# Kernel tuning notes

Measured on AMD Instinct MI355X. Metric: run time of the kernel, lower is better.

The kernel has to match this reference:

```python
import jax, jax.numpy as jnp
import numpy as np

RADIUS, HMIN, HMAX, NSAMPLE = 0.05, -0.02, 0.04, 32
EPS = 1e-5


def setup_inputs() -> dict:
    key = jax.random.key(0)
    ks = jax.random.split(key, 6)
    B, N, C, OUT = 4, 2048, 256, 256
    seed_xyz_graspable = jax.random.uniform(ks[0], (B, N, 3), jnp.float32) * 0.2
    seed_features_graspable = jax.random.normal(ks[1], (B, C, N), jnp.float32)
    vp_rot = jax.random.normal(ks[2], (B, N, 3, 3), jnp.float32)
    W1 = jax.random.normal(ks[3], (OUT, 3 + C), jnp.float32) * 0.02
    W2 = jax.random.normal(ks[4], (OUT, OUT), jnp.float32) * 0.02
    return {
        "seed_xyz_graspable": seed_xyz_graspable,
        "seed_features_graspable": seed_features_graspable,
        "vp_rot": vp_rot,
        "W1": W1, "gamma1": jnp.ones((OUT,), jnp.float32), "beta1": jnp.zeros((OUT,), jnp.float32),
        "W2": W2, "gamma2": jnp.ones((OUT,), jnp.float32), "beta2": jnp.zeros((OUT,), jnp.float32),
    }


def _cylinder_query(xyz, rot):
    # xyz: (B,N,3), rot: (B,N,3,3); new_xyz == xyz.
    B, N, _ = xyz.shape
    d = xyz[:, None, :, :] - xyz[:, :, None, :]                  # (B,P,N,3) offsets to each candidate
    r = jnp.einsum('bpij,bpnj->bpni', rot, d)                    # rotate into cylinder frame (rot @ d)
    mask = (r[..., 1] ** 2 + r[..., 2] ** 2 < RADIUS ** 2) & (r[..., 0] > HMIN) & (r[..., 0] < HMAX)
    order = jnp.arange(N, dtype=jnp.int32)
    keys = jnp.where(mask, order, order + N)                     # in-cylinder points sort first, stable order
    _, idx = jax.lax.top_k(-keys, NSAMPLE)                       # first NSAMPLE indices satisfying the query
    valid = jnp.take_along_axis(mask, idx, axis=-1)
    first = idx[..., :1]
    any_valid = valid[..., :1]
    idx = jnp.where(valid, idx, jnp.where(any_valid, first, 0))  # pad with first hit like the CUDA kernel
    return idx                                                   # (B,P,NSAMPLE) int32


def _group(xyz, features, rot, idx):
    gxyz = jax.vmap(lambda a, i: a[i])(xyz, idx)                 # (B,P,S,3)
    gxyz = (gxyz - xyz[:, :, None, :]) / RADIUS                  # center on query + normalize_xyz
    gxyz = jnp.einsum('bpsj,bpjk->bpsk', gxyz, rot)              # rotate_xyz: grouped_xyz @ rot
    gfeat = jax.vmap(lambda f, i: f[:, i])(features, idx)        # (B,C,P,S)
    return jnp.concatenate([gxyz.transpose(0, 3, 1, 2), gfeat], axis=1)  # (B,3+C,P,S)


def _conv_bn_relu(x, W, gamma, beta):
    y = jnp.einsum('oc,bcps->bops', W, x)                        # 1x1 conv, no bias (bn=True)
    mu = y.mean(axis=(0, 2, 3), keepdims=True)
    var = y.var(axis=(0, 2, 3), keepdims=True)
    y = (y - mu) * jax.lax.rsqrt(var + EPS)
    y = y * gamma[None, :, None, None] + beta[None, :, None, None]
    return jax.nn.relu(y)


def reference(seed_xyz_graspable, seed_features_graspable, vp_rot, W1, gamma1, beta1, W2, gamma2, beta2):
    idx = _cylinder_query(seed_xyz_graspable, vp_rot)
    g = _group(seed_xyz_graspable, seed_features_graspable, vp_rot, idx)
    h = _conv_bn_relu(g, W1, gamma1, beta1)
    h = _conv_bn_relu(h, W2, gamma2, beta2)
    return h.max(axis=3)                                         # maxpool over nsample -> (B,OUT,P)
```

## Files before the change

kernel.cpp:

```cpp
#include <hip/hip_runtime.h>

typedef unsigned short u16;
typedef unsigned int u32;
typedef __attribute__((ext_vector_type(8))) short bf16x8;
typedef __attribute__((ext_vector_type(4))) float f32x4;

#define NPTS 2048
#define CFEAT 256
#define NS 32
#define MTOT 262144
#define NBLK 4096
#define INV_N (1.0f/262144.0f)

__device__ __forceinline__ float bf2f(u16 u) {
    union { u32 i; float f; } v; v.i = ((u32)u) << 16; return v.f;
}
__device__ __forceinline__ u16 f2bf(float f) {
    union { float f; u32 i; } v; v.f = f;
    u32 i = v.i;
    return (u16)((i + 0x7fffu + ((i >> 16) & 1u)) >> 16);
}
__device__ __forceinline__ u32 pk2bf(float a, float b) {
    u32 r;
    asm("v_cvt_pk_bf16_f32 %0, %1, %2" : "=v"(r) : "v"(a), "v"(b));
    return r;
}

__device__ __forceinline__ void gload16(const void* g, void* l) {
    __builtin_amdgcn_global_load_lds((const __attribute__((address_space(1))) void*)g,
                                     (__attribute__((address_space(3))) void*)l, 16, 0, 0);
}

__global__ __launch_bounds__(256) void query_k(const float* __restrict__ xyz, const float* __restrict__ rot,
                                               const float* __restrict__ feat,
                                               int* __restrict__ idx, u16* __restrict__ gxyz,
                                               u16* __restrict__ featT,
                                               const float* __restrict__ W1, const float* __restrict__ W2,
                                               u16* __restrict__ Wp1, u16* __restrict__ Wp2) {
    __shared__ float sm[32 * 33];
    __shared__ float xbs[NPTS * 3];
    __shared__ int sidx[4 * NS];
    const int tid = threadIdx.x;
    if (blockIdx.x < 256) {
        int o = blockIdx.x;
        Wp1[o * 288 + tid] = f2bf(W1[o * 259 + 3 + tid]);
        if (tid < 32) Wp1[o * 288 + 256 + tid] = (tid < 3) ? f2bf(W1[o * 259 + tid]) : (u16)0;
        Wp2[o * 256 + tid] = f2bf(W2[o * 256 + tid]);
    }
    const int b = blockIdx.x >> 9;
    const float* xb = xyz + (size_t)b * NPTS * 3;
    const int c0 = ((blockIdx.x >> 6) & 7) * 32;
    const int n0f = (blockIdx.x & 63) * 32;
    {
        int x = tid & 31, y = tid >> 5;
        #pragma unroll
        for (int rr = 0; rr < 4; rr++) {
            int c = c0 + y + rr * 8;
            sm[(y + rr * 8) * 33 + x] = feat[((size_t)(b * CFEAT + c)) * NPTS + n0f + x];
        }
    }
    {
        const uint4* src = (const uint4*)xb;
        uint4* dst = (uint4*)xbs;
        #pragma unroll
        for (int u = 0; u < 6; u++) dst[u * 256 + tid] = src[u * 256 + tid];
    }
    __syncthreads();
    {
        int x = tid & 31, y = tid >> 5;
        #pragma unroll
        for (int rr = 0; rr < 4; rr++) {
            int n = n0f + y + rr * 8;
            featT[((size_t)(b * NPTS + n)) * CFEAT + c0 + x] = (u16)pk2bf(sm[x * 33 + (y + rr * 8)], 0.f);
        }
    }
    const int wid = tid >> 6;
    const int pid = blockIdx.x * 4 + wid;
    const int lane = tid & 63;
    const int p = pid & 2047;
    float px = xbs[p * 3 + 0], py = xbs[p * 3 + 1], pz = xbs[p * 3 + 2];
    const float* rp = rot + (size_t)pid * 9;
    float r00 = rp[0], r01 = rp[1], r02 = rp[2];
    float r10 = rp[3], r11 = rp[4], r12 = rp[5];
    float r20 = rp[6], r21 = rp[7], r22 = rp[8];
    int cnt = 0, first = 0;
    for (int n0 = 0; n0 < NPTS && cnt < NS; n0 += 64) {
        int n = n0 + lane;
        float dx = __fsub_rn(xbs[n * 3 + 0], px);
        float dy = __fsub_rn(xbs[n * 3 + 1], py);
        float dz = __fsub_rn(xbs[n * 3 + 2], pz);
        float a0 = __fadd_rn(__fadd_rn(__fmul_rn(r00, dx), __fmul_rn(r01, dy)), __fmul_rn(r02, dz));
        float a1 = __fadd_rn(__fadd_rn(__fmul_rn(r10, dx), __fmul_rn(r11, dy)), __fmul_rn(r12, dz));
        float a2 = __fadd_rn(__fadd_rn(__fmul_rn(r20, dx), __fmul_rn(r21, dy)), __fmul_rn(r22, dz));
        float t2 = __fadd_rn(__fmul_rn(a1, a1), __fmul_rn(a2, a2));
        bool valid = (t2 < 0.0025f) && (a0 > -0.02f) && (a0 < 0.04f);
        unsigned long long bal = __ballot(valid);
        if (cnt == 0 && bal) first = n0 + __builtin_ctzll(bal);
        int rank = __builtin_popcountll(bal & ((1ull << lane) - 1ull));
        int slot = cnt + rank;
        if (valid && slot < NS) sidx[wid * NS + slot] = n;
        cnt += __builtin_popcountll(bal);
    }
    int filled = cnt < NS ? cnt : NS;
    __syncthreads();
    if (lane < NS) {
        int i = (lane < filled) ? sidx[wid * NS + lane] : (cnt > 0 ? first : 0);
        idx[(size_t)pid * NS + lane] = i;
        float dx = (xbs[i * 3 + 0] - px) * 20.0f;
        float dy = (xbs[i * 3 + 1] - py) * 20.0f;
        float dz = (xbs[i * 3 + 2] - pz) * 20.0f;
        float g0 = dx * r00 + dy * r10 + dz * r20;
        float g1 = dx * r01 + dy * r11 + dz * r21;
        float g2 = dx * r02 + dy * r12 + dz * r22;
        uint2 v;
        v.x = pk2bf(g0, g1);
        v.y = pk2bf(g2, 0.f);
        *(uint2*)(gxyz + ((size_t)pid * NS + lane) * 4) = v;
    }
}

template <int FULL, int STORE>
__global__ __launch_bounds__(256) void fused_k(
    const u16* __restrict__ featT, const u16* __restrict__ gxyz, const int* __restrict__ idx,
    const u16* __restrict__ Wp1, const u16* __restrict__ Wp2, const float* __restrict__ ab1,
    float* __restrict__ psum, float* __restrict__ psq,
    float* __restrict__ ymax, float* __restrict__ ymin, uint2* __restrict__ y1f)
{
    __shared__ __attribute__((aligned(16))) u16 As[64 * 64];
    __shared__ __attribute__((aligned(16))) u16 Bs[256 * 64];
    __shared__ __attribute__((aligned(16))) u16 y1s[FULL ? 64 * 264 : 16];
    __shared__ int rowbase_s[64];

    const int tid = threadIdx.x;
    const int lane = tid & 63, wave = tid >> 6;
    const int quad = lane >> 4, tl = lane & 15;
    const int bx = blockIdx.x;
    const int m0 = bx * 64;

    if (tid < 64) {
        int m = m0 + tid;
        int gi = idx[m];
        int b = m >> 16;
        rowbase_s[tid] = (b * NPTS + gi) * CFEAT;
    }
    __syncthreads();

    const int sr8 = tid >> 3;
    const int koffA = (((tid & 7) ^ (sr8 & 7)) * 8);

    f32x4 acc[4][4];
    #pragma unroll
    for (int i = 0; i < 4; i++)
        #pragma unroll
        for (int j = 0; j < 4; j++) acc[i][j] = (f32x4){0.f, 0.f, 0.f, 0.f};

    for (int t = 0; t < 4; t++) {
        const int k0 = t * 64;
        __syncthreads();
        gload16(featT + rowbase_s[sr8] + k0 + koffA, As + tid * 8);
        gload16(featT + rowbase_s[sr8 + 32] + k0 + koffA, As + 2048 + tid * 8);
        #pragma unroll
        for (int c = 0; c < 8; c++)
            gload16(Wp1 + (c * 32 + sr8) * 288 + k0 + koffA, Bs + c * 2048 + tid * 8);
        __syncthreads();
        #pragma unroll
        for (int kk = 0; kk < 2; kk++) {
            bf16x8 af[4], bv[4];
            #pragma unroll
            for (int i = 0; i < 4; i++)
                af[i] = *(const bf16x8*)(As + (i * 16 + tl) * 64 + (((kk * 4 + quad) ^ (tl & 7)) * 8));
            #pragma unroll
            for (int j = 0; j < 4; j++)
                bv[j] = *(const bf16x8*)(Bs + (j * 64 + wave * 16 + tl) * 64 + (((kk * 4 + quad) ^ (tl & 7)) * 8));
            #pragma unroll
            for (int i = 0; i < 4; i++)
                #pragma unroll
                for (int j = 0; j < 4; j++)
                    acc[i][j] = __builtin_amdgcn_mfma_f32_16x16x32_bf16(af[i], bv[j], acc[i][j], 0, 0, 0);
        }
    }
    {
        __syncthreads();
        const int srow = tid >> 2, sc16 = tid & 3;
        uint4 va = make_uint4(0, 0, 0, 0);
        if (sc16 == 0) {
            uint2 g2 = *(const uint2*)(gxyz + (size_t)(m0 + srow) * 4);
            va.x = g2.x; va.y = g2.y;
        }
        *(uint4*)(As + srow * 64 + ((sc16 ^ (srow & 7)) * 8)) = va;
        #pragma unroll
        for (int s = 0; s < 4; s++) {
            uint4 w = *(const uint4*)(Wp1 + tid * 288 + 256 + s * 8);
            *(uint4*)(Bs + tid * 64 + ((s ^ (tid & 7)) * 8)) = w;
        }
        __syncthreads();
        bf16x8 af[4], bv[4];
        #pragma unroll
        for (int i = 0; i < 4; i++)
            af[i] = *(const bf16x8*)(As + (i * 16 + tl) * 64 + ((quad ^ (tl & 7)) * 8));
        #pragma unroll
        for (int j = 0; j < 4; j++)
            bv[j] = *(const bf16x8*)(Bs + (j * 64 + wave * 16 + tl) * 64 + ((quad ^ (tl & 7)) * 8));
        #pragma unroll
        for (int i = 0; i < 4; i++)
            #pragma unroll
            for (int j = 0; j < 4; j++)
                acc[i][j] = __builtin_amdgcn_mfma_f32_16x16x32_bf16(af[i], bv[j], acc[i][j], 0, 0, 0);
    }

    if (!FULL) {
        #pragma unroll
        for (int j = 0; j < 4; j++) {
            float s = 0.f, q2 = 0.f;
            #pragma unroll
            for (int i = 0; i < 4; i++) {
                float v0 = acc[i][j][0], v1 = acc[i][j][1], v2 = acc[i][j][2], v3 = acc[i][j][3];
                if (STORE) {
                    u32 lo = pk2bf(v0, v1);
                    u32 hi = pk2bf(v2, v3);
                    y1f[((size_t)(bx * 4 + wave) * 16 + i * 4 + j) * 64 + lane] = make_uint2(lo, hi);
                    v0 = bf2f((u16)(lo & 0xffff)); v1 = bf2f((u16)(lo >> 16));
                    v2 = bf2f((u16)(hi & 0xffff)); v3 = bf2f((u16)(hi >> 16));
                }
                s += v0 + v1 + v2 + v3;
                q2 += v0 * v0 + v1 * v1 + v2 * v2 + v3 * v3;
            }
            s += __shfl_xor(s, 16); s += __shfl_xor(s, 32);
            q2 += __shfl_xor(q2, 16); q2 += __shfl_xor(q2, 32);
            if (quad == 0) {
                int col = j * 64 + wave * 16 + tl;
                psum[(size_t)bx * 256 + col] = s;
                psq[(size_t)bx * 256 + col] = q2;
            }
        }
        return;
    }

    #pragma unroll
    for (int j = 0; j < 4; j++) {
        int col = j * 64 + wave * 16 + tl;
        float a = ab1[col], bb = ab1[256 + col];
        #pragma unroll
        for (int i = 0; i < 4; i++)
            #pragma unroll
            for (int r = 0; r < 4; r++) {
                float v = fmaxf(fmaf(acc[i][j][r], a, bb), 0.f);
                y1s[(i * 16 + quad * 4 + r) * 264 + col] = f2bf(v);
            }
    }

    const int srow = tid >> 2, sc16 = tid & 3;
    f32x4 acc2[4][4];
    #pragma unroll
    for (int i = 0; i < 4; i++)
        #pragma unroll
        for (int j = 0; j < 4; j++) acc2[i][j] = (f32x4){0.f, 0.f, 0.f, 0.f};
    for (int ks = 0; ks < 8; ks++) {
        const int k0 = ks * 32;
        __syncthreads();
        #pragma unroll
        for (int q = 0; q < 4; q++)
            gload16(Wp2 + (srow + q * 64) * 256 + k0 + sc16 * 8, Bs + q * 2048 + tid * 8);
        __syncthreads();
        bf16x8 af[4], bv[4];
        #pragma unroll
        for (int i = 0; i < 4; i++) af[i] = *(const bf16x8*)(y1s + (i * 16 + tl) * 264 + k0 + quad * 8);
        #pragma unroll
        for (int j = 0; j < 4; j++) bv[j] = *(const bf16x8*)(Bs + (j * 64 + wave * 16 + tl) * 32 + quad * 8);
        #pragma unroll
        for (int i = 0; i < 4; i++)
            #pragma unroll
            for (int j = 0; j < 4; j++)
                acc2[i][j] = __builtin_amdgcn_mfma_f32_16x16x32_bf16(af[i], bv[j], acc2[i][j], 0, 0, 0);
    }

    #pragma unroll
    for (int j = 0; j < 4; j++) {
        int col = j * 64 + wave * 16 + tl;
        float s = 0.f, q2 = 0.f;
        float mx0 = -3.0e38f, mn0 = 3.0e38f, mx1 = -3.0e38f, mn1 = 3.0e38f;
        #pragma unroll
        for (int i = 0; i < 4; i++)
            #pragma unroll
            for (int r = 0; r < 4; r++) {
                float v = acc2[i][j][r];
                s += v; q2 += v * v;
                if (i < 2) { mx0 = fmaxf(mx0, v); mn0 = fminf(mn0, v); }
                else       { mx1 = fmaxf(mx1, v); mn1 = fminf(mn1, v); }
            }
        s += __shfl_xor(s, 16); s += __shfl_xor(s, 32);
        q2 += __shfl_xor(q2, 16); q2 += __shfl_xor(q2, 32);
        mx0 = fmaxf(mx0, __shfl_xor(mx0, 16)); mx0 = fmaxf(mx0, __shfl_xor(mx0, 32));
        mn0 = fminf(mn0, __shfl_xor(mn0, 16)); mn0 = fminf(mn0, __shfl_xor(mn0, 32));
        mx1 = fmaxf(mx1, __shfl_xor(mx1, 16)); mx1 = fmaxf(mx1, __shfl_xor(mx1, 32));
        mn1 = fminf(mn1, __shfl_xor(mn1, 16)); mn1 = fminf(mn1, __shfl_xor(mn1, 32));
        if (quad == 0) {
            psum[(size_t)bx * 256 + col] = s;
            psq[(size_t)bx * 256 + col] = q2;
            size_t p0 = (size_t)(bx * 2) * 256 + col;
            size_t p1 = (size_t)(bx * 2 + 1) * 256 + col;
            ymax[p0] = mx0; ymin[p0] = mn0;
            ymax[p1] = mx1; ymin[p1] = mn1;
        }
    }
}

__global__ __launch_bounds__(256) void fused2_k(
    const uint2* __restrict__ y1f, const u16* __restrict__ Wp2, const float* __restrict__ ab1,
    float* __restrict__ psum, float* __restrict__ psq,
    float* __restrict__ ymax, float* __restrict__ ymin)
{
    __shared__ __attribute__((aligned(16))) u16 Bs[256 * 64];
    __shared__ __attribute__((aligned(16))) u16 y1s[64 * 136];
    const int tid = threadIdx.x;
    const int lane = tid & 63, wave = tid >> 6;
    const int quad = lane >> 4, tl = lane & 15;
    const int bx = blockIdx.x;
    const int sr8 = tid >> 3;
    const int koffB = (((tid & 7) ^ (sr8 & 7)) * 8);

    float yv[4][4][4];
    #pragma unroll
    for (int j = 0; j < 4; j++) {
        int col = j * 64 + wave * 16 + tl;
        float a = ab1[col], bb = ab1[256 + col];
        #pragma unroll
        for (int i = 0; i < 4; i++) {
            uint2 v = y1f[((size_t)(bx * 4 + wave) * 16 + i * 4 + j) * 64 + lane];
            yv[j][i][0] = fmaxf(fmaf(bf2f((u16)(v.x & 0xffff)), a, bb), 0.f);
            yv[j][i][1] = fmaxf(fmaf(bf2f((u16)(v.x >> 16)), a, bb), 0.f);
            yv[j][i][2] = fmaxf(fmaf(bf2f((u16)(v.y & 0xffff)), a, bb), 0.f);
            yv[j][i][3] = fmaxf(fmaf(bf2f((u16)(v.y >> 16)), a, bb), 0.f);
        }
    }
    #pragma unroll
    for (int j = 0; j < 2; j++) {
        int col = j * 64 + wave * 16 + tl;
        #pragma unroll
        for (int i = 0; i < 4; i++)
            #pragma unroll
            for (int r = 0; r < 4; r++)
                y1s[(i * 16 + quad * 4 + r) * 136 + col] = (u16)pk2bf(yv[j][i][r], 0.f);
    }

    f32x4 acc2[4][4];
    #pragma unroll
    for (int i = 0; i < 4; i++)
        #pragma unroll
        for (int j = 0; j < 4; j++) acc2[i][j] = (f32x4){0.f, 0.f, 0.f, 0.f};

    for (int t = 0; t < 4; t++) {
        const int k0 = t * 64;
        __syncthreads();
        if (t == 2) {
            #pragma unroll
            for (int j = 2; j < 4; j++) {
                int lc = (j - 2) * 64 + wave * 16 + tl;
                #pragma unroll
                for (int i = 0; i < 4; i++)
                    #pragma unroll
                    for (int r = 0; r < 4; r++)
                        y1s[(i * 16 + quad * 4 + r) * 136 + lc] = (u16)pk2bf(yv[j][i][r], 0.f);
            }
        }
        #pragma unroll
        for (int c = 0; c < 8; c++)
            gload16(Wp2 + (c * 32 + sr8) * 256 + k0 + koffB, Bs + c * 2048 + tid * 8);
        __syncthreads();
        const int klb = (t & 1) * 64;
        #pragma unroll
        for (int kk = 0; kk < 2; kk++) {
            bf16x8 af[4], bv[4];
            #pragma unroll
            for (int i = 0; i < 4; i++)
                af[i] = *(const bf16x8*)(y1s + (i * 16 + tl) * 136 + klb + kk * 32 + quad * 8);
            #pragma unroll
            for (int j = 0; j < 4; j++)
                bv[j] = *(const bf16x8*)(Bs + (j * 64 + wave * 16 + tl) * 64 + (((kk * 4 + quad) ^ (tl & 7)) * 8));
            #pragma unroll
            for (int i = 0; i < 4; i++)
                #pragma unroll
                for (int j = 0; j < 4; j++)
                    acc2[i][j] = __builtin_amdgcn_mfma_f32_16x16x32_bf16(af[i], bv[j], acc2[i][j], 0, 0, 0);
        }
    }

    #pragma unroll
    for (int j = 0; j < 4; j++) {
        int col = j * 64 + wave * 16 + tl;
        float s = 0.f, q2 = 0.f;
        float mx0 = -3.0e38f, mn0 = 3.0e38f, mx1 = -3.0e38f, mn1 = 3.0e38f;
        #pragma unroll
        for (int i = 0; i < 4; i++)
            #pragma unroll
            for (int r = 0; r < 4; r++) {
                float v = acc2[i][j][r];
                s += v; q2 += v * v;
                if (i < 2) { mx0 = fmaxf(mx0, v); mn0 = fminf(mn0, v); }
                else       { mx1 = fmaxf(mx1, v); mn1 = fminf(mn1, v); }
            }
        s += __shfl_xor(s, 16); s += __shfl_xor(s, 32);
        q2 += __shfl_xor(q2, 16); q2 += __shfl_xor(q2, 32);
        mx0 = fmaxf(mx0, __shfl_xor(mx0, 16)); mx0 = fmaxf(mx0, __shfl_xor(mx0, 32));
        mn0 = fminf(mn0, __shfl_xor(mn0, 16)); mn0 = fminf(mn0, __shfl_xor(mn0, 32));
        mx1 = fmaxf(mx1, __shfl_xor(mx1, 16)); mx1 = fmaxf(mx1, __shfl_xor(mx1, 32));
        mn1 = fminf(mn1, __shfl_xor(mn1, 16)); mn1 = fminf(mn1, __shfl_xor(mn1, 32));
        if (quad == 0) {
            psum[(size_t)bx * 256 + col] = s;
            psq[(size_t)bx * 256 + col] = q2;
            size_t p0 = (size_t)(bx * 2) * 256 + col;
            size_t p1 = (size_t)(bx * 2 + 1) * 256 + col;
            ymax[p0] = mx0; ymin[p0] = mn0;
            ymax[p1] = mx1; ymin[p1] = mn1;
        }
    }
}

__global__ __launch_bounds__(256) void reduce1_k(const float* __restrict__ psum, const float* __restrict__ psq,
                                                 float* __restrict__ ps2, float* __restrict__ pq2) {
    int j = blockIdx.x, t = threadIdx.x;
    float s = 0.f, q = 0.f;
    #pragma unroll 4
    for (int kk = 0; kk < 64; kk++) {
        size_t r = (size_t)(j * 64 + kk) * 256 + t;
        s += psum[r]; q += psq[r];
    }
    ps2[j * 256 + t] = s;
    pq2[j * 256 + t] = q;
}

__global__ __launch_bounds__(256) void reduce2_k(const float* __restrict__ ps2, const float* __restrict__ pq2,
                                                 const float* __restrict__ gamma, const float* __restrict__ beta,
                                                 float* __restrict__ ab) {
    int c = threadIdx.x;
    float S = 0.f, Q = 0.f;
    for (int j = 0; j < 64; j++) {
        S += ps2[j * 256 + c];
        Q += pq2[j * 256 + c];
    }
    float mu = S * INV_N;
    float var = Q * INV_N - mu * mu;
    float a = gamma[c] * rsqrtf(var + 1e-5f);
    ab[c] = a;
    ab[256 + c] = beta[c] - mu * a;
}

__global__ __launch_bounds__(256) void final_k(const float* __restrict__ ymax, const float* __restrict__ ymin,
                                               const float* __restrict__ ab, float* __restrict__ out) {
    __shared__ float sm[32 * 33];
    int b = blockIdx.z;
    int n0 = blockIdx.x * 32, o0 = blockIdx.y * 32;
    int t = threadIdx.x, x = t & 31, y = t >> 5;
    #pragma unroll
    for (int rr = 0; rr < 4; rr++) {
        int n = n0 + y + rr * 8;
        int o = o0 + x;
        float a = ab[o], bb = ab[256 + o];
        size_t p = (size_t)(b * NPTS + n) * 256 + o;
        float v = (a >= 0.f) ? ymax[p] : ymin[p];
        sm[(y + rr * 8) * 33 + x] = fmaxf(fmaf(v, a, bb), 0.f);
    }
    __syncthreads();
    #pragma unroll
    for (int rr = 0; rr < 4; rr++)
        out[((size_t)(b * 256 + o0 + y + rr * 8)) * NPTS + n0 + x] = sm[x * 33 + (y + rr * 8)];
}

extern "C" void kernel_launch(void* const* d_in, const int* in_sizes, int n_in,
                              void* d_out, int out_size, void* d_ws, size_t ws_size,
                              hipStream_t stream) {
    const float* xyz    = (const float*)d_in[0];
    const float* feat   = (const float*)d_in[1];
    const float* rot    = (const float*)d_in[2];
    const float* W1     = (const float*)d_in[3];
    const float* gamma1 = (const float*)d_in[4];
    const float* beta1  = (const float*)d_in[5];
    const float* W2     = (const float*)d_in[6];
    const float* gamma2 = (const float*)d_in[7];
    const float* beta2  = (const float*)d_in[8];
    float* out = (float*)d_out;

    char* ws = (char*)d_ws;
    u16*   featT = (u16*)(ws + 0);
    int*   idxp  = (int*)(ws + 4194304);
    u16*   gxyz  = (u16*)(ws + 5242880);
    u16*   Wp1   = (u16*)(ws + 7340032);
    u16*   Wp2   = (u16*)(ws + 7487488);
    float* ab1   = (float*)(ws + 7618560);
    float* ab2   = (float*)(ws + 7620608);
    float* psum  = (float*)(ws + 7622656);
    float* psq   = (float*)(ws + 11816960);
    float* ymax  = (float*)(ws + 16011264);
    float* ymin  = (float*)(ws + 24399872);
    uint2* y1f   = (uint2*)(ws + 32788480);
    const size_t BIG_NEED = 32788480ull + 134217728ull;

    float* r1s = (float*)(ws + 24399872);
    float* r1q = r1s + 16384;
    float* r2s = (float*)(ws + 5242880);
    float* r2q = r2s + 16384;

    query_k<<<2048, 256, 0, stream>>>(xyz, rot, feat, idxp, gxyz, featT, W1, W2, Wp1, Wp2);

    if (ws_size >= BIG_NEED) {
        fused_k<0, 1><<<NBLK, 256, 0, stream>>>(featT, gxyz, idxp, Wp1, Wp2, ab1, psum, psq, ymax, ymin, y1f);
        reduce1_k<<<64, 256, 0, stream>>>(psum, psq, r1s, r1q);
        reduce2_k<<<1, 256, 0, stream>>>(r1s, r1q, gamma1, beta1, ab1);
        fused2_k<<<NBLK, 256, 0, stream>>>(y1f, Wp2, ab1, psum, psq, ymax, ymin);
        reduce1_k<<<64, 256, 0, stream>>>(psum, psq, r2s, r2q);
        reduce2_k<<<1, 256, 0, stream>>>(r2s, r2q, gamma2, beta2, ab2);
    } else {
        fused_k<0, 0><<<NBLK, 256, 0, stream>>>(featT, gxyz, idxp, Wp1, Wp2, ab1, psum, psq, ymax, ymin, nullptr);
        reduce1_k<<<64, 256, 0, stream>>>(psum, psq, r1s, r1q);
        reduce2_k<<<1, 256, 0, stream>>>(r1s, r1q, gamma1, beta1, ab1);
        fused_k<1, 0><<<NBLK, 256, 0, stream>>>(featT, gxyz, idxp, Wp1, Wp2, ab1, psum, psq, ymax, ymin, nullptr);
        reduce1_k<<<64, 256, 0, stream>>>(psum, psq, r2s, r2q);
        reduce2_k<<<1, 256, 0, stream>>>(r2s, r2q, gamma2, beta2, ab2);
    }
    final_k<<<dim3(64, 8, 4), 256, 0, stream>>>(ymax, ymin, ab2, out);
}
```

Baseline: 228.8 us.

## Compute BN1 statistics from per-point GEMM with gather histogram instead of full pass

BN1 statistics are computed algebraically. A histogram counts how often each source point is gathered and sums its grouped xyz. A small GEMM over the 8192 unique points (instead of 262144 grouped rows) then weights the feature projection by those counts, and cross terms with the xyz part come from second moments. The separate first-pass kernel and its large bf16 intermediate buffer are dropped. A single fused kernel recomputes layer 1 and runs layer 2 with a smaller shared-memory footprint. The risks are float atomics in shared memory and precision loss in the var = E[x²] − mu² form.

```diff
diff --git a/kernel.cpp b/kernel.cpp
--- a/kernel.cpp
+++ b/kernel.cpp
@@ -10,6 +10,7 @@
 #define NS 32
 #define MTOT 262144
 #define NBLK 4096
+#define NROW 8192
 #define INV_N (1.0f/262144.0f)
 
 __device__ __forceinline__ float bf2f(u16 u) {
@@ -119,17 +120,161 @@
     }
 }
 
-template <int FULL, int STORE>
-__global__ __launch_bounds__(256) void fused_k(
+__global__ __launch_bounds__(256) void hist_k(const int* __restrict__ idx, const u16* __restrict__ gxyz,
+                                              float* __restrict__ hpart, float* __restrict__ xst64,
+                                              float* __restrict__ Sacc) {
+    __shared__ float hist[8192];
+    __shared__ float red[9 * 4];
+    const int t = threadIdx.x, lane = t & 63, wave = t >> 6;
+    const int g = blockIdx.x;
+    const int base = g * 4096;
+    if (g == 0) { Sacc[t] = 0.f; Sacc[t + 256] = 0.f; Sacc[t + 512] = 0.f; }
+    for (int i = t; i < 8192; i += 256) hist[i] = 0.f;
+    __syncthreads();
+    float p[9] = {0.f,0.f,0.f,0.f,0.f,0.f,0.f,0.f,0.f};
+    for (int u = 0; u < 16; u++) {
+        int m = base + u * 256 + t;
+        int r = idx[m];
+        uint2 v = *(const uint2*)(gxyz + (size_t)m * 4);
+        float x0 = bf2f((u16)(v.x & 0xffff));
+        float x1 = bf2f((u16)(v.x >> 16));
+        float x2 = bf2f((u16)(v.y & 0xffff));
+        atomicAdd(hist + r * 4 + 0, 1.f);
+        atomicAdd(hist + r * 4 + 1, x0);
+        atomicAdd(hist + r * 4 + 2, x1);
+        atomicAdd(hist + r * 4 + 3, x2);
+        p[0] += x0; p[1] += x1; p[2] += x2;
+        p[3] += x0 * x0; p[4] += x0 * x1; p[5] += x0 * x2;
+        p[6] += x1 * x1; p[7] += x1 * x2; p[8] += x2 * x2;
+    }
+    __syncthreads();
+    for (int i = t; i < 8192; i += 256) hpart[(size_t)g * 8192 + i] = hist[i];
+    #pragma unroll
+    for (int k = 0; k < 9; k++) {
+        float s = p[k];
+        #pragma unroll
+        for (int o = 1; o < 64; o <<= 1) s += __shfl_xor(s, o);
+        if (lane == 0) red[k * 4 + wave] = s;
+    }
+    __syncthreads();
+    if (t < 9) xst64[g * 9 + t] = red[t * 4 + 0] + red[t * 4 + 1] + red[t * 4 + 2] + red[t * 4 + 3];
+}
+
+__global__ __launch_bounds__(256) void zgemm_k(const u16* __restrict__ featT, const u16* __restrict__ Wp1,
+                                               const float* __restrict__ hpart,
+                                               float* __restrict__ Sacc, float* __restrict__ Qacc,
+                                               float* __restrict__ Xacc) {
+    __shared__ __attribute__((aligned(16))) u16 As[64 * 32];
+    __shared__ __attribute__((aligned(16))) u16 Bs[256 * 32];
+    __shared__ float cxs[64 * 4];
+    const int tid = threadIdx.x;
+    const int lane = tid & 63, wave = tid >> 6;
+    const int quad = lane >> 4, tl = lane & 15;
+    const int m0 = blockIdx.x * 64;
+    const int srow = tid >> 2, sc16 = tid & 3;
+    const int abase = (m0 + srow) * CFEAT + sc16 * 8;
+
+    {
+        const int b = m0 >> 11;
+        const int rl0 = m0 & 2047;
+        int row = tid >> 2, c = tid & 3;
+        float s = 0.f;
+        #pragma unroll
+        for (int sg = 0; sg < 16; sg++)
+            s += hpart[(size_t)(b * 16 + sg) * 8192 + (rl0 + row) * 4 + c];
+        cxs[tid] = s;
+    }
+
+    f32x4 acc[4][4];
+    #pragma unroll
+    for (int i = 0; i < 4; i++)
+        #pragma unroll
+        for (int j = 0; j < 4; j++) acc[i][j] = (f32x4){0.f, 0.f, 0.f, 0.f};
+
+    for (int ks = 0; ks < 8; ks++) {
+        const int k0 = ks * 32;
+        __syncthreads();
+        gload16(featT + abase + k0, As + tid * 8);
+        #pragma unroll
+        for (int q = 0; q < 4; q++)
+            gload16(Wp1 + (srow + q * 64) * 288 + k0 + sc16 * 8, Bs + q * 2048 + tid * 8);
+        __syncthreads();
+        bf16x8 af[4], bv[4];
+        #pragma unroll
+        for (int i = 0; i < 4; i++) af[i] = *(const bf16x8*)(As + (i * 16 + tl) * 32 + quad * 8);
+        #pragma unroll
+        for (int j = 0; j < 4; j++) bv[j] = *(const bf16x8*)(Bs + (wave * 64 + j * 16 + tl) * 32 + quad * 8);
+        #pragma unroll
+        for (int i = 0; i < 4; i++)
+            #pragma unroll
+            for (int j = 0; j < 4; j++)
+                acc[i][j] = __builtin_amdgcn_mfma_f32_16x16x32_bf16(af[i], bv[j], acc[i][j], 0, 0, 0);
+    }
+
+    #pragma unroll
+    for (int j = 0; j < 4; j++) {
+        int col = wave * 64 + j * 16 + tl;
+        float wx0 = bf2f(Wp1[col * 288 + 256]);
+        float wx1 = bf2f(Wp1[col * 288 + 257]);
+        float wx2 = bf2f(Wp1[col * 288 + 258]);
+        float S = 0.f, Q = 0.f, X = 0.f;
+        #pragma unroll
+        for (int i = 0; i < 4; i++)
+            #pragma unroll
+            for (int rr = 0; rr < 4; rr++) {
+                int row = i * 16 + quad * 4 + rr;
+                float4 cx = *(const float4*)(cxs + row * 4);
+                float z = acc[i][j][rr];
+                S += cx.x * z;
+                Q += cx.x * z * z;
+                X += z * (wx0 * cx.y + wx1 * cx.z + wx2 * cx.w);
+            }
+        S += __shfl_xor(S, 16); S += __shfl_xor(S, 32);
+        Q += __shfl_xor(Q, 16); Q += __shfl_xor(Q, 32);
+        X += __shfl_xor(X, 16); X += __shfl_xor(X, 32);
+        if (quad == 0) {
+            atomicAdd(Sacc + col, S);
+            atomicAdd(Qacc + col, Q);
+            atomicAdd(Xacc + col, X);
+        }
+    }
+}
+
+__global__ __launch_bounds__(256) void ab1_k(const float* __restrict__ Sacc, const float* __restrict__ Qacc,
+                                             const float* __restrict__ Xacc, const float* __restrict__ xst64,
+                                             const u16* __restrict__ Wp1,
+                                             const float* __restrict__ gamma, const float* __restrict__ beta,
+                                             float* __restrict__ ab) {
+    int c = threadIdx.x;
+    float xs[9] = {0.f,0.f,0.f,0.f,0.f,0.f,0.f,0.f,0.f};
+    for (int g = 0; g < 64; g++)
+        #pragma unroll
+        for (int k = 0; k < 9; k++) xs[k] += xst64[g * 9 + k];
+    float wx0 = bf2f(Wp1[c * 288 + 256]);
+    float wx1 = bf2f(Wp1[c * 288 + 257]);
+    float wx2 = bf2f(Wp1[c * 288 + 258]);
+    float S = Sacc[c] + wx0 * xs[0] + wx1 * xs[1] + wx2 * xs[2];
+    float qxx = wx0 * wx0 * xs[3] + wx1 * wx1 * xs[6] + wx2 * wx2 * xs[8]
+              + 2.f * (wx0 * wx1 * xs[4] + wx0 * wx2 * xs[5] + wx1 * wx2 * xs[7]);
+    float Q = Qacc[c] + 2.f * Xacc[c] + qxx;
+    float mu = S * INV_N;
+    float var = Q * INV_N - mu * mu;
+    float a = gamma[c] * rsqrtf(var + 1e-5f);
+    ab[c] = a;
+    ab[256 + c] = beta[c] - mu * a;
+}
+
+__global__ __launch_bounds__(256) void full_k(
     const u16* __restrict__ featT, const u16* __restrict__ gxyz, const int* __restrict__ idx,
     const u16* __restrict__ Wp1, const u16* __restrict__ Wp2, const float* __restrict__ ab1,
     float* __restrict__ psum, float* __restrict__ psq,
-    float* __restrict__ ymax, float* __restrict__ ymin, uint2* __restrict__ y1f)
+    float* __restrict__ ymax, float* __restrict__ ymin)
 {
-    __shared__ __attribute__((aligned(16))) u16 As[64 * 64];
     __shared__ __attribute__((aligned(16))) u16 Bs[256 * 64];
-    __shared__ __attribute__((aligned(16))) u16 y1s[FULL ? 64 * 264 : 16];
+    __shared__ __attribute__((aligned(16))) u16 AY[64 * 136];
     __shared__ int rowbase_s[64];
+    u16* As = AY;
+    u16* y1s = AY;
 
     const int tid = threadIdx.x;
     const int lane = tid & 63, wave = tid >> 6;
@@ -207,71 +352,60 @@
             for (int j = 0; j < 4; j++)
                 acc[i][j] = __builtin_amdgcn_mfma_f32_16x16x32_bf16(af[i], bv[j], acc[i][j], 0, 0, 0);
     }
-
-    if (!FULL) {
-        #pragma unroll
-        for (int j = 0; j < 4; j++) {
-            float s = 0.f, q2 = 0.f;
-            #pragma unroll
-            for (int i = 0; i < 4; i++) {
-                float v0 = acc[i][j][0], v1 = acc[i][j][1], v2 = acc[i][j][2], v3 = acc[i][j][3];
-                if (STORE) {
-                    u32 lo = pk2bf(v0, v1);
-                    u32 hi = pk2bf(v2, v3);
-                    y1f[((size_t)(bx * 4 + wave) * 16 + i * 4 + j) * 64 + lane] = make_uint2(lo, hi);
-                    v0 = bf2f((u16)(lo & 0xffff)); v1 = bf2f((u16)(lo >> 16));
-                    v2 = bf2f((u16)(hi & 0xffff)); v3 = bf2f((u16)(hi >> 16));
-                }
-                s += v0 + v1 + v2 + v3;
-                q2 += v0 * v0 + v1 * v1 + v2 * v2 + v3 * v3;
-            }
-            s += __shfl_xor(s, 16); s += __shfl_xor(s, 32);
-            q2 += __shfl_xor(q2, 16); q2 += __shfl_xor(q2, 32);
-            if (quad == 0) {
-                int col = j * 64 + wave * 16 + tl;
-                psum[(size_t)bx * 256 + col] = s;
-                psq[(size_t)bx * 256 + col] = q2;
-            }
-        }
-        return;
-    }
-
-    #pragma unroll
-    for (int j = 0; j < 4; j++) {
+    __syncthreads();
+
+    #pragma unroll
+    for (int j = 0; j < 2; j++) {
         int col = j * 64 + wave * 16 + tl;
         float a = ab1[col], bb = ab1[256 + col];
         #pragma unroll
         for (int i = 0; i < 4; i++)
             #pragma unroll
-            for (int r = 0; r < 4; r++) {
-                float v = fmaxf(fmaf(acc[i][j][r], a, bb), 0.f);
-                y1s[(i * 16 + quad * 4 + r) * 264 + col] = f2bf(v);
+            for (int r = 0; r < 4; r++)
+                y1s[(i * 16 + quad * 4 + r) * 136 + col] = (u16)pk2bf(fmaxf(fmaf(acc[i][j][r], a, bb), 0.f), 0.f);
+    }
+
+    f32x4 acc2[4][4];
+    #pragma unroll
+    for (int i = 0; i < 4; i++)
+        #pragma unroll
+        for (int j = 0; j < 4; j++) acc2[i][j] = (f32x4){0.f, 0.f, 0.f, 0.f};
+    for (int t = 0; t < 4; t++) {
+        const int k0 = t * 64;
+        __syncthreads();
+        if (t == 2) {
+            #pragma unroll
+            for (int j = 2; j < 4; j++) {
+                int col = j * 64 + wave * 16 + tl;
+                int lc = col - 128;
+                float a = ab1[col], bb = ab1[256 + col];
+                #pragma unroll
+                for (int i = 0; i < 4; i++)
+                    #pragma unroll
+                    for (int r = 0; r < 4; r++)
+                        y1s[(i * 16 + quad * 4 + r) * 136 + lc] = (u16)pk2bf(fmaxf(fmaf(acc[i][j][r], a, bb), 0.f), 0.f);
             }
-    }
-
-    const int srow = tid >> 2, sc16 = tid & 3;
-    f32x4 acc2[4][4];
-    #pragma unroll
-    for (int i = 0; i < 4; i++)
-        #pragma unroll
-        for (int j = 0; j < 4; j++) acc2[i][j] = (f32x4){0.f, 0.f, 0.f, 0.f};
-    for (int ks = 0; ks < 8; ks++) {
-        const int k0 = ks * 32;
-        __syncthreads();
-        #pragma unroll
-        for (int q = 0; q < 4; q++)
-            gload16(Wp2 + (srow + q * 64) * 256 + k0 + sc16 * 8, Bs + q * 2048 + tid * 8);
-        __syncthreads();
-        bf16x8 af[4], bv[4];
-        #pragma unroll
-        for (int i = 0; i < 4; i++) af[i] = *(const bf16x8*)(y1s + (i * 16 + tl) * 264 + k0 + quad * 8);
-        #pragma unroll
-        for (int j = 0; j < 4; j++) bv[j] = *(const bf16x8*)(Bs + (j * 64 + wave * 16 + tl) * 32 + quad * 8);
-        #pragma unroll
-        for (int i = 0; i < 4; i++)
+        }
+        #pragma unroll
+        for (int c = 0; c < 8; c++)
+            gload16(Wp2 + (c * 32 + sr8) * 256 + k0 + koffA, Bs + c * 2048 + tid * 8);
+        __syncthreads();
+        const int klb = (t & 1) * 64;
+        #pragma unroll
+        for (int kk = 0; kk < 2; kk++) {
+            bf16x8 af[4], bv[4];
+            #pragma unroll
+            for (int i = 0; i < 4; i++)
+                af[i] = *(const bf16x8*)(y1s + (i * 16 + tl) * 136 + klb + kk * 32 + quad * 8);
             #pragma unroll
             for (int j = 0; j < 4; j++)
-                acc2[i][j] = __builtin_amdgcn_mfma_f32_16x16x32_bf16(af[i], bv[j], acc2[i][j], 0, 0, 0);
+                bv[j] = *(const bf16x8*)(Bs + (j * 64 + wave * 16 + tl) * 64 + (((kk * 4 + quad) ^ (tl & 7)) * 8));
+            #pragma unroll
+            for (int i = 0; i < 4; i++)
+                #pragma unroll
+                for (int j = 0; j < 4; j++)
+                    acc2[i][j] = __builtin_amdgcn_mfma_f32_16x16x32_bf16(af[i], bv[j], acc2[i][j], 0, 0, 0);
+        }
     }
 
     #pragma unroll
@@ -305,84 +439,152 @@
     }
 }
 
-__global__ __launch_bounds__(256) void fused2_k(
-    const uint2* __restrict__ y1f, const u16* __restrict__ Wp2, const float* __restrict__ ab1,
+template <int FULL, int STORE>
+__global__ __launch_bounds__(256) void fused_k(
+    const u16* __restrict__ featT, const u16* __restrict__ gxyz, const int* __restrict__ idx,
+    const u16* __restrict__ Wp1, const u16* __restrict__ Wp2, const float* __restrict__ ab1,
     float* __restrict__ psum, float* __restrict__ psq,
-    float* __restrict__ ymax, float* __restrict__ ymin)
+    float* __restrict__ ymax, float* __restrict__ ymin, uint2* __restrict__ y1f)
 {
+    __shared__ __attribute__((aligned(16))) u16 As[64 * 64];
     __shared__ __attribute__((aligned(16))) u16 Bs[256 * 64];
-    __shared__ __attribute__((aligned(16))) u16 y1s[64 * 136];
+    __shared__ __attribute__((aligned(16))) u16 y1s[FULL ? 64 * 264 : 16];
+    __shared__ int rowbase_s[64];
+
     const int tid = threadIdx.x;
     const int lane = tid & 63, wave = tid >> 6;
     const int quad = lane >> 4, tl = lane & 15;
     const int bx = blockIdx.x;
+    const int m0 = bx * 64;
+
+    if (tid < 64) {
+        int m = m0 + tid;
+        int gi = idx[m];
+        int b = m >> 16;
+        rowbase_s[tid] = (b * NPTS + gi) * CFEAT;
+    }
+    __syncthreads();
+
     const int sr8 = tid >> 3;
-    const int koffB = (((tid & 7) ^ (sr8 & 7)) * 8);
-
-    float yv[4][4][4];
+    const int koffA = (((tid & 7) ^ (sr8 & 7)) * 8);
+
+    f32x4 acc[4][4];
+    #pragma unroll
+    for (int i = 0; i < 4; i++)
+        #pragma unroll
+        for (int j = 0; j < 4; j++) acc[i][j] = (f32x4){0.f, 0.f, 0.f, 0.f};
+
+    for (int t = 0; t < 4; t++) {
+        const int k0 = t * 64;
+        __syncthreads();
+        gload16(featT + rowbase_s[sr8] + k0 + koffA, As + tid * 8);
+        gload16(featT + rowbase_s[sr8 + 32] + k0 + koffA, As + 2048 + tid * 8);
+        #pragma unroll
+        for (int c = 0; c < 8; c++)
+            gload16(Wp1 + (c * 32 + sr8) * 288 + k0 + koffA, Bs + c * 2048 + tid * 8);
+        __syncthreads();
+        #pragma unroll
+        for (int kk = 0; kk < 2; kk++) {
+            bf16x8 af[4], bv[4];
+            #pragma unroll
+            for (int i = 0; i < 4; i++)
+                af[i] = *(const bf16x8*)(As + (i * 16 + tl) * 64 + (((kk * 4 + quad) ^ (tl & 7)) * 8));
+            #pragma unroll
+            for (int j = 0; j < 4; j++)
+                bv[j] = *(const bf16x8*)(Bs + (j * 64 + wave * 16 + tl) * 64 + (((kk * 4 + quad) ^ (tl & 7)) * 8));
+            #pragma unroll
+            for (int i = 0; i < 4; i++)
+                #pragma unroll
+                for (int j = 0; j < 4; j++)
+                    acc[i][j] = __builtin_amdgcn_mfma_f32_16x16x32_bf16(af[i], bv[j], acc[i][j], 0, 0, 0);
+        }
+    }
+    {
+        __syncthreads();
+        const int srow = tid >> 2, sc16 = tid & 3;
+        uint4 va = make_uint4(0, 0, 0, 0);
+        if (sc16 == 0) {
+            uint2 g2 = *(const uint2*)(gxyz + (size_t)(m0 + srow) * 4);
+            va.x = g2.x; va.y = g2.y;
+        }
+        *(uint4*)(As + srow * 64 + ((sc16 ^ (srow & 7)) * 8)) = va;
+        #pragma unroll
+        for (int s = 0; s < 4; s++) {
+            uint4 w = *(const uint4*)(Wp1 + tid * 288 + 256 + s * 8);
+            *(uint4*)(Bs + tid * 64 + ((s ^ (tid & 7)) * 8)) = w;
+        }
+        __syncthreads();
+        bf16x8 af[4], bv[4];
+        #pragma unroll
+        for (int i = 0; i < 4; i++)
+            af[i] = *(const bf16x8*)(As + (i * 16 + tl) * 64 + ((quad ^ (tl & 7)) * 8));
+        #pragma unroll
+        for (int j = 0; j < 4; j++)
+            bv[j] = *(const bf16x8*)(Bs + (j * 64 + wave * 16 + tl) * 64 + ((quad ^ (tl & 7)) * 8));
+        #pragma unroll
+        for (int i = 0; i < 4; i++)
+            #pragma unroll
+            for (int j = 0; j < 4; j++)
+                acc[i][j] = __builtin_amdgcn_mfma_f32_16x16x32_bf16(af[i], bv[j], acc[i][j], 0, 0, 0);
+    }
+
+    if (!FULL) {
+        #pragma unroll
+        for (int j = 0; j < 4; j++) {
+            float s = 0.f, q2 = 0.f;
+            #pragma unroll
+            for (int i = 0; i < 4; i++) {
+                float v0 = acc[i][j][0], v1 = acc[i][j][1], v2 = acc[i][j][2], v3 = acc[i][j][3];
+                s += v0 + v1 + v2 + v3;
+                q2 += v0 * v0 + v1 * v1 + v2 * v2 + v3 * v3;
+            }
+            s += __shfl_xor(s, 16); s += __shfl_xor(s, 32);
+            q2 += __shfl_xor(q2, 16); q2 += __shfl_xor(q2, 32);
+            if (quad == 0) {
+                int col = j * 64 + wave * 16 + tl;
+                psum[(size_t)bx * 256 + col] = s;
+                psq[(size_t)bx * 256 + col] = q2;
+            }
+        }
+        return;
+    }
+
     #pragma unroll
     for (int j = 0; j < 4; j++) {
         int col = j * 64 + wave * 16 + tl;
         float a = ab1[col], bb = ab1[256 + col];
         #pragma unroll
-        for (int i = 0; i < 4; i++) {
-            uint2 v = y1f[((size_t)(bx * 4 + wave) * 16 + i * 4 + j) * 64 + lane];
-            yv[j][i][0] = fmaxf(fmaf(bf2f((u16)(v.x & 0xffff)), a, bb), 0.f);
-            yv[j][i][1] = fmaxf(fmaf(bf2f((u16)(v.x >> 16)), a, bb), 0.f);
-            yv[j][i][2] = fmaxf(fmaf(bf2f((u16)(v.y & 0xffff)), a, bb), 0.f);
-            yv[j][i][3] = fmaxf(fmaf(bf2f((u16)(v.y >> 16)), a, bb), 0.f);
-        }
-    }
-    #pragma unroll
-    for (int j = 0; j < 2; j++) {
-        int col = j * 64 + wave * 16 + tl;
-        #pragma unroll
-        for (int i = 0; i < 4; i++)
-            #pragma unroll
-            for (int r = 0; r < 4; r++)
-                y1s[(i * 16 + quad * 4 + r) * 136 + col] = (u16)pk2bf(yv[j][i][r], 0.f);
-    }
-
+        for (int i = 0; i < 4; i++)
+            #pragma unroll
+            for (int r = 0; r < 4; r++) {
+                float v = fmaxf(fmaf(acc[i][j][r], a, bb), 0.f);
+                y1s[(i * 16 + quad * 4 + r) * 264 + col] = f2bf(v);
+            }
+    }
+
+    const int srow = tid >> 2, sc16 = tid & 3;
     f32x4 acc2[4][4];
     #pragma unroll
     for (int i = 0; i < 4; i++)
         #pragma unroll
         for (int j = 0; j < 4; j++) acc2[i][j] = (f32x4){0.f, 0.f, 0.f, 0.f};
-
-    for (int t = 0; t < 4; t++) {
-        const int k0 = t * 64;
-        __syncthreads();
-        if (t == 2) {
-            #pragma unroll
-            for (int j = 2; j < 4; j++) {
-                int lc = (j - 2) * 64 + wave * 16 + tl;
-                #pragma unroll
-                for (int i = 0; i < 4; i++)
-                    #pragma unroll
-                    for (int r = 0; r < 4; r++)
-                        y1s[(i * 16 + quad * 4 + r) * 136 + lc] = (u16)pk2bf(yv[j][i][r], 0.f);
-            }
-        }
-        #pragma unroll
-        for (int c = 0; c < 8; c++)
-            gload16(Wp2 + (c * 32 + sr8) * 256 + k0 + koffB, Bs + c * 2048 + tid * 8);
-        __syncthreads();
-        const int klb = (t & 1) * 64;
-        #pragma unroll
-        for (int kk = 0; kk < 2; kk++) {
-            bf16x8 af[4], bv[4];
-            #pragma unroll
-            for (int i = 0; i < 4; i++)
-                af[i] = *(const bf16x8*)(y1s + (i * 16 + tl) * 136 + klb + kk * 32 + quad * 8);
+    for (int ks = 0; ks < 8; ks++) {
+        const int k0 = ks * 32;
+        __syncthreads();
+        #pragma unroll
+        for (int q = 0; q < 4; q++)
+            gload16(Wp2 + (srow + q * 64) * 256 + k0 + sc16 * 8, Bs + q * 2048 + tid * 8);
+        __syncthreads();
+        bf16x8 af[4], bv[4];
+        #pragma unroll
+        for (int i = 0; i < 4; i++) af[i] = *(const bf16x8*)(y1s + (i * 16 + tl) * 264 + k0 + quad * 8);
+        #pragma unroll
+        for (int j = 0; j < 4; j++) bv[j] = *(const bf16x8*)(Bs + (j * 64 + wave * 16 + tl) * 32 + quad * 8);
+        #pragma unroll
+        for (int i = 0; i < 4; i++)
             #pragma unroll
             for (int j = 0; j < 4; j++)
-                bv[j] = *(const bf16x8*)(Bs + (j * 64 + wave * 16 + tl) * 64 + (((kk * 4 + quad) ^ (tl & 7)) * 8));
-            #pragma unroll
-            for (int i = 0; i < 4; i++)
-                #pragma unroll
-                for (int j = 0; j < 4; j++)
-                    acc2[i][j] = __builtin_amdgcn_mfma_f32_16x16x32_bf16(af[i], bv[j], acc2[i][j], 0, 0, 0);
-        }
+                acc2[i][j] = __builtin_amdgcn_mfma_f32_16x16x32_bf16(af[i], bv[j], acc2[i][j], 0, 0, 0);
     }
 
     #pragma unroll
@@ -492,8 +694,12 @@
     float* psq   = (float*)(ws + 11816960);
     float* ymax  = (float*)(ws + 16011264);
     float* ymin  = (float*)(ws + 24399872);
-    uint2* y1f   = (uint2*)(ws + 32788480);
-    const size_t BIG_NEED = 32788480ull + 134217728ull;
+    float* hpart = (float*)(ws + 32788480);
+    float* Sacc  = (float*)(ws + 34885632);
+    float* Qacc  = (float*)(ws + 34886656);
+    float* Xacc  = (float*)(ws + 34887680);
+    float* xst64 = (float*)(ws + 34888704);
+    const size_t BIG_NEED = 34892800ull;
 
     float* r1s = (float*)(ws + 24399872);
     float* r1q = r1s + 16384;
@@ -503,10 +709,10 @@
     query_k<<<2048, 256, 0, stream>>>(xyz, rot, feat, idxp, gxyz, featT, W1, W2, Wp1, Wp2);
 
     if (ws_size >= BIG_NEED) {
-        fused_k<0, 1><<<NBLK, 256, 0, stream>>>(featT, gxyz, idxp, Wp1, Wp2, ab1, psum, psq, ymax, ymin, y1f);
-        reduce1_k<<<64, 256, 0, stream>>>(psum, psq, r1s, r1q);
-        reduce2_k<<<1, 256, 0, stream>>>(r1s, r1q, gamma1, beta1, ab1);
-        fused2_k<<<NBLK, 256, 0, stream>>>(y1f, Wp2, ab1, psum, psq, ymax, ymin);
+        hist_k<<<64, 256, 0, stream>>>(idxp, gxyz, hpart, xst64, Sacc);
+        zgemm_k<<<NROW / 64, 256, 0, stream>>>(featT, Wp1, hpart, Sacc, Qacc, Xacc);
+        ab1_k<<<1, 256, 0, stream>>>(Sacc, Qacc, Xacc, xst64, Wp1, gamma1, beta1, ab1);
+        full_k<<<NBLK, 256, 0, stream>>>(featT, gxyz, idxp, Wp1, Wp2, ab1, psum, psq, ymax, ymin);
         reduce1_k<<<64, 256, 0, stream>>>(psum, psq, r2s, r2q);
         reduce2_k<<<1, 256, 0, stream>>>(r2s, r2q, gamma2, beta2, ab2);
     } else {
```

Result: slower. 262.1 us (+14.5%).
